# Optimization experiments

Measured on AMD Instinct MI355X. Metric: run time of the kernel, lower is better.

The kernel has to match this reference:

```python
import jax, jax.numpy as jnp
import numpy as np

B, L, S, N, D, DT, V, H = 32, 256, 5, 1024, 256, 256, 512, 8
Dh = D // H


def layernorm(x, g, b, eps=1e-5):
    m = x.mean(-1, keepdims=True)
    v = ((x - m) ** 2).mean(-1, keepdims=True)
    return (x - m) / jnp.sqrt(v + eps) * g + b


def setup_inputs() -> dict:
    key = jax.random.key(0)
    ks = jax.random.split(key, 16)
    sc = lambda k, shape: jax.random.normal(k, shape, jnp.float32) * 0.02
    return {
        'vis_tokens': jax.random.normal(ks[0], (B, N, D), jnp.float32),
        'left_ctx_ids': jax.random.randint(ks[1], (B, L, S), 0, V),
        'right_ctx_ids': jax.random.randint(ks[2], (B, L, S), 0, V),
        'tgt_ids': jax.random.randint(ks[3], (B, L), 0, V),
        'tgt_mask': jnp.ones((B, L), jnp.float32),
        'vis_mask': jax.random.uniform(ks[4], (B, L, N), jnp.float32),
        'emb_w': sc(ks[5], (V, DT)),          # tied embedding / classifier weight
        'dir_left': sc(ks[6], (DT,)),
        'dir_right': sc(ks[7], (DT,)),
        'txt_proj_w': sc(ks[8], (D, DT)), 'txt_proj_b': jnp.zeros((D,), jnp.float32),
        'q_gamma': jnp.ones((D,), jnp.float32), 'q_beta': jnp.zeros((D,), jnp.float32),
        'k_w': sc(ks[9], (D, D)), 'k_b': jnp.zeros((D,), jnp.float32),
        'v_w': sc(ks[10], (D, D)), 'v_b': jnp.zeros((D,), jnp.float32),
        'kv_gamma': jnp.ones((D,), jnp.float32), 'kv_beta': jnp.zeros((D,), jnp.float32),
        'tau': jnp.asarray(1.0, jnp.float32),
        'cls_b': jnp.zeros((V,), jnp.float32),
        'conv_w_l': sc(ks[11], (DT, DT, 3)),   # fresh random conv weight per call in torch
        'conv_w_r': sc(ks[12], (DT, DT, 3)),
    }


def _ctx_to_query(ctx_ids, dir_tok, conv_w, emb_w, txt_proj_w, txt_proj_b, qg, qb):
    E = emb_w[ctx_ids]                                    # [B,L,S,DT]
    q = jnp.transpose(E, (0, 1, 3, 2)).reshape(B * L, DT, S)
    q = jax.lax.conv_general_dilated(q, conv_w, (1,), [(1, 1)],
                                     dimension_numbers=('NCH', 'OIH', 'NCH'))  # [B*L,DT,S]
    # faithful to torch: flat reinterpretation [B*L,DT,S] -> [B,L,S,DT], then mean over dim 2
    q = q.reshape(B, L, -1, DT).mean(2)                   # [B,L,DT]
    q = q + dir_tok
    return layernorm(q @ txt_proj_w.T + txt_proj_b, qg, qb)  # [B,L,D]


def _cross_attend(Q, Fv, vis_mask, k_w, k_b, v_w, v_b, kvg, kvb, tau):
    K = layernorm(Fv @ k_w.T + k_b, kvg, kvb)             # [B,N,D]
    Vv = layernorm(Fv @ v_w.T + v_b, kvg, kvb)
    q = Q.reshape(B, L, H, Dh).transpose(0, 2, 1, 3)      # [B,H,L,Dh]
    k = K.reshape(B, N, H, Dh).transpose(0, 2, 1, 3)
    v = Vv.reshape(B, N, H, Dh).transpose(0, 2, 1, 3)
    tau_c = jnp.clip(tau, 0.25, 4.0)
    scores = jnp.einsum('bhld,bhnd->bhln', q, k) / (Dh ** 0.5 * tau_c)
    scores = scores * vis_mask[:, None]                   # multiplicative mask
    attn = jax.nn.softmax(scores, axis=-1)                # dropout = identity (eval)
    out = jnp.einsum('bhln,bhnd->bhld', attn, v)
    return out.transpose(0, 2, 1, 3).reshape(B, L, D)


def reference(vis_tokens, left_ctx_ids, right_ctx_ids, tgt_ids, tgt_mask, vis_mask,
              emb_w, dir_left, dir_right, txt_proj_w, txt_proj_b, q_gamma, q_beta,
              k_w, k_b, v_w, v_b, kv_gamma, kv_beta, tau, cls_b, conv_w_l, conv_w_r):
    Ql = _ctx_to_query(left_ctx_ids, dir_left, conv_w_l, emb_w, txt_proj_w, txt_proj_b, q_gamma, q_beta)
    Qr = _ctx_to_query(right_ctx_ids, dir_right, conv_w_r, emb_w, txt_proj_w, txt_proj_b, q_gamma, q_beta)
    Fl = _cross_attend(Ql, vis_tokens, vis_mask, k_w, k_b, v_w, v_b, kv_gamma, kv_beta, tau)
    Fr = _cross_attend(Qr, vis_tokens, vis_mask, k_w, k_b, v_w, v_b, kv_gamma, kv_beta, tau)
    logits_l = Fl @ emb_w.T + cls_b                       # tied classifier
    logits_r = Fr @ emb_w.T + cls_b
    p_l = jax.nn.softmax(logits_l / 2.0, axis=-1)
    p_r = jax.nn.softmax(logits_r / 2.0, axis=-1)
    agree = ((p_l[:, :-1, :] - p_r[:, 1:, :]) ** 2).sum(-1)
    denom = jnp.maximum(tgt_mask[:, :-1].sum(), 1.0)
    loss_sgm = 0.1 * (agree * tgt_mask[:, :-1]).sum() / denom
    return loss_sgm, logits_l, logits_r
```

## Files before the change

### kernel.cpp

```cpp
#include <hip/hip_runtime.h>

typedef __attribute__((ext_vector_type(8))) short short8;
typedef __attribute__((ext_vector_type(4))) short short4v;
typedef __attribute__((ext_vector_type(4))) float f32x4;

__device__ __forceinline__ short f2bf(float x) {
    union { float f; unsigned u; } c; c.f = x;
    unsigned u = c.u;
    u += 0x7fffu + ((u >> 16) & 1u);
    return (short)(u >> 16);
}

__global__ __launch_bounds__(256) void cvt_bf16(const float* __restrict__ s, short* __restrict__ d, int n4) {
    int i = blockIdx.x * 256 + threadIdx.x;
    if (i < n4) {
        float4 v = ((const float4*)s)[i];
        short4 o;
        o.x = f2bf(v.x); o.y = f2bf(v.y); o.z = f2bf(v.z); o.w = f2bf(v.w);
        ((short4*)d)[i] = o;
    }
}

__global__ __launch_bounds__(256) void cvt3(const float* __restrict__ emb, const float* __restrict__ kw,
                                            const float* __restrict__ vw,
                                            short* __restrict__ de, short* __restrict__ dk, short* __restrict__ dv) {
    int i = blockIdx.x * 256 + threadIdx.x;
    const float* s; short* d; int off;
    if (i < 32768) { s = emb; d = de; off = i; }
    else if (i < 49152) { s = kw; d = dk; off = i - 32768; }
    else { s = vw; d = dv; off = i - 49152; }
    float4 v = ((const float4*)s)[off];
    short4 o;
    o.x = f2bf(v.x); o.y = f2bf(v.y); o.z = f2bf(v.z); o.w = f2bf(v.w);
    ((short4*)d)[off] = o;
}

__global__ void build_wfold(const float* __restrict__ cl, const float* __restrict__ cr,
                            float* __restrict__ wfT) {
    const float* conv_w = blockIdx.y ? cr : cl;
    float* o = wfT + (long)blockIdx.y * 327680;
    const int j = blockIdx.x;
    const int ci = threadIdx.x;
    float acc[5] = {0.f, 0.f, 0.f, 0.f, 0.f};
#pragma unroll
    for (int i = 0; i < 5; ++i) {
        int flat = i * 256 + j;
        int c = flat / 5;
        int s = flat % 5;
#pragma unroll
        for (int k = 0; k < 3; ++k) {
            int si = s + k - 1;
            if (si >= 0 && si < 5) acc[si] += conv_w[(c * 256 + ci) * 3 + k];
        }
    }
#pragma unroll
    for (int si = 0; si < 5; ++si)
        o[(si * 256 + ci) * 256 + j] = acc[si] * 0.2f;
}

template <bool BIAS>
__global__ __launch_bounds__(256) void gemm64(const float* __restrict__ A,
                                              const float* __restrict__ W,
                                              const float* __restrict__ bias,
                                              float* __restrict__ C,
                                              int K, int ldC,
                                              long sliceA, long sliceW, long sliceC) {
    A += (long)blockIdx.z * sliceA;
    W += (long)blockIdx.z * sliceW;
    C += (long)blockIdx.z * sliceC;
    const int row0 = blockIdx.x * 64;
    const int col0 = blockIdx.y * 64;
    __shared__ float As[32][68];
    __shared__ float Ws[32][68];
    const int t = threadIdx.x;
    const int tx = t & 15;
    const int ty = t >> 4;
    float acc[4][4] = {};
    for (int kk = 0; kk < K; kk += 32) {
#pragma unroll
        for (int e = 0; e < 8; ++e) {
            int f = t + 256 * e;
            int r = f >> 5, kc = f & 31;
            As[kc][r] = A[(long)(row0 + r) * K + kk + kc];
            Ws[kc][r] = W[(long)(col0 + r) * K + kk + kc];
        }
        __syncthreads();
#pragma unroll
        for (int kc = 0; kc < 32; ++kc) {
            float4 a4 = *(const float4*)&As[kc][ty * 4];
            float4 w4 = *(const float4*)&Ws[kc][tx * 4];
            float av[4] = {a4.x, a4.y, a4.z, a4.w};
            float wv[4] = {w4.x, w4.y, w4.z, w4.w};
#pragma unroll
            for (int i = 0; i < 4; ++i)
#pragma unroll
                for (int jj = 0; jj < 4; ++jj)
                    acc[i][jj] += av[i] * wv[jj];
        }
        __syncthreads();
    }
#pragma unroll
    for (int r = 0; r < 4; ++r) {
        int row = row0 + ty * 4 + r;
#pragma unroll
        for (int c = 0; c < 4; ++c) {
            int col = col0 + tx * 4 + c;
            float v = acc[r][c];
            if (BIAS) v += bias[col];
            C[(long)row * ldC + col] = v;
        }
    }
}

__global__ __launch_bounds__(256) void gemm_bf(const short* __restrict__ A,
                                               const short* __restrict__ W,
                                               const float* __restrict__ bias,
                                               float* __restrict__ Cf,
                                               int K, int ldC,
                                               long sliceA, long sliceC) {
    A += (long)blockIdx.z * sliceA;
    const int row0 = blockIdx.x * 64, col0 = blockIdx.y * 64;
    __shared__ short As[64 * 40];
    __shared__ short Ws[64 * 40];
    const int t = threadIdx.x;
    const int wid = t >> 6, lane = t & 63, sub = lane & 15, quad = lane >> 4;
    const int wy = wid >> 1, wx = wid & 1;
    const int srow = t >> 2, sseg = t & 3;
    f32x4 acc00 = {0.f, 0.f, 0.f, 0.f}, acc01 = acc00, acc10 = acc00, acc11 = acc00;
    for (int kk = 0; kk < K; kk += 32) {
        *(short8*)&As[srow * 40 + sseg * 8] = *(const short8*)&A[(long)(row0 + srow) * K + kk + sseg * 8];
        *(short8*)&Ws[srow * 40 + sseg * 8] = *(const short8*)&W[(long)(col0 + srow) * K + kk + sseg * 8];
        __syncthreads();
        short8 a0 = *(const short8*)&As[(wy * 32 + sub) * 40 + quad * 8];
        short8 a1 = *(const short8*)&As[(wy * 32 + 16 + sub) * 40 + quad * 8];
        short8 b0 = *(const short8*)&Ws[(wx * 32 + sub) * 40 + quad * 8];
        short8 b1 = *(const short8*)&Ws[(wx * 32 + 16 + sub) * 40 + quad * 8];
        acc00 = __builtin_amdgcn_mfma_f32_16x16x32_bf16(a0, b0, acc00, 0, 0, 0);
        acc01 = __builtin_amdgcn_mfma_f32_16x16x32_bf16(a0, b1, acc01, 0, 0, 0);
        acc10 = __builtin_amdgcn_mfma_f32_16x16x32_bf16(a1, b0, acc10, 0, 0, 0);
        acc11 = __builtin_amdgcn_mfma_f32_16x16x32_bf16(a1, b1, acc11, 0, 0, 0);
        __syncthreads();
    }
    Cf += (long)blockIdx.z * sliceC;
#pragma unroll
    for (int i = 0; i < 2; ++i)
#pragma unroll
        for (int j = 0; j < 2; ++j) {
            f32x4 a = (i == 0) ? (j == 0 ? acc00 : acc01) : (j == 0 ? acc10 : acc11);
#pragma unroll
            for (int r = 0; r < 4; ++r) {
                int row = row0 + wy * 32 + i * 16 + quad * 4 + r;
                int col = col0 + wx * 32 + j * 16 + sub;
                Cf[(long)row * ldC + col] = a[r] + bias[col];
            }
        }
}

__global__ __launch_bounds__(256) void gemm_ln(const short* __restrict__ A,
                                               const short* __restrict__ kwbf, const short* __restrict__ vwbf,
                                               const float* __restrict__ k_b, const float* __restrict__ v_b,
                                               const float* __restrict__ gamma, const float* __restrict__ beta,
                                               short* __restrict__ Kout, short* __restrict__ Vt) {
    const bool isV = blockIdx.y != 0;
    const short* W = isV ? vwbf : kwbf;
    const float* bias = isV ? v_b : k_b;
    const int row0 = blockIdx.x * 64;
    __shared__ short As[64 * 40];
    __shared__ short Ws[256 * 40];
    __shared__ float s_mu[64 * 4];
    __shared__ float s_sq[64 * 4];
    __shared__ float s_mv[64 * 2];
    const int t = threadIdx.x;
    const int wid = t >> 6, lane = t & 63, sub = lane & 15, quad = lane >> 4;
    f32x4 acc[4][4];
#pragma unroll
    for (int mi = 0; mi < 4; ++mi)
#pragma unroll
        for (int ni = 0; ni < 4; ++ni) acc[mi][ni] = (f32x4){0.f, 0.f, 0.f, 0.f};

    const int sr = t >> 2, sseg = t & 3;
    for (int kk = 0; kk < 256; kk += 32) {
        *(short8*)&As[sr * 40 + sseg * 8] = *(const short8*)&A[(long)(row0 + sr) * 256 + kk + sseg * 8];
#pragma unroll
        for (int i = 0; i < 4; ++i) {
            int r = i * 64 + sr;
            *(short8*)&Ws[r * 40 + sseg * 8] = *(const short8*)&W[(long)r * 256 + kk + sseg * 8];
        }
        __syncthreads();
        short8 a[4], b[4];
#pragma unroll
        for (int mi = 0; mi < 4; ++mi) a[mi] = *(const short8*)&As[(mi * 16 + sub) * 40 + quad * 8];
#pragma unroll
        for (int ni = 0; ni < 4; ++ni) b[ni] = *(const short8*)&Ws[(wid * 64 + ni * 16 + sub) * 40 + quad * 8];
#pragma unroll
        for (int mi = 0; mi < 4; ++mi)
#pragma unroll
            for (int ni = 0; ni < 4; ++ni)
                acc[mi][ni] = __builtin_amdgcn_mfma_f32_16x16x32_bf16(a[mi], b[ni], acc[mi][ni], 0, 0, 0);
        __syncthreads();
    }
#pragma unroll
    for (int ni = 0; ni < 4; ++ni) {
        float bv = bias[wid * 64 + ni * 16 + sub];
#pragma unroll
        for (int mi = 0; mi < 4; ++mi)
#pragma unroll
            for (int r = 0; r < 4; ++r) acc[mi][ni][r] += bv;
    }
#pragma unroll
    for (int mi = 0; mi < 4; ++mi) {
#pragma unroll
        for (int r = 0; r < 4; ++r) {
            float s = 0.f, q2 = 0.f;
#pragma unroll
            for (int ni = 0; ni < 4; ++ni) {
                float v = acc[mi][ni][r];
                s += v; q2 += v * v;
            }
#pragma unroll
            for (int off = 8; off; off >>= 1) {
                s += __shfl_xor(s, off, 16);
                q2 += __shfl_xor(q2, off, 16);
            }
            if (sub == 0) {
                int row = mi * 16 + quad * 4 + r;
                s_mu[row * 4 + wid] = s;
                s_sq[row * 4 + wid] = q2;
            }
        }
    }
    __syncthreads();
    if (t < 64) {
        float s = s_mu[t * 4] + s_mu[t * 4 + 1] + s_mu[t * 4 + 2] + s_mu[t * 4 + 3];
        float q2 = s_sq[t * 4] + s_sq[t * 4 + 1] + s_sq[t * 4 + 2] + s_sq[t * 4 + 3];
        float mean = s * (1.0f / 256.0f);
        float var = q2 * (1.0f / 256.0f) - mean * mean;
        s_mv[t * 2] = mean;
        s_mv[t * 2 + 1] = rsqrtf(var + 1e-5f);
    }
    __syncthreads();
#pragma unroll
    for (int ni = 0; ni < 4; ++ni) {
        int col = wid * 64 + ni * 16 + sub;
        float g = gamma[col], bb = beta[col];
        if (!isV) {
#pragma unroll
            for (int mi = 0; mi < 4; ++mi)
#pragma unroll
                for (int r = 0; r < 4; ++r) {
                    int row = mi * 16 + quad * 4 + r;
                    float v = (acc[mi][ni][r] - s_mv[row * 2]) * s_mv[row * 2 + 1] * g + bb;
                    Kout[(long)(row0 + row) * 256 + col] = f2bf(v);
                }
        } else {
            int h = col >> 5, dh = col & 31;
#pragma unroll
            for (int mi = 0; mi < 4; ++mi) {
                int rowb = row0 + mi * 16 + quad * 4;
                short4 o;
#pragma unroll
                for (int r = 0; r < 4; ++r) {
                    int row = mi * 16 + quad * 4 + r;
                    float v = (acc[mi][ni][r] - s_mv[row * 2]) * s_mv[row * 2 + 1] * g + bb;
                    ((short*)&o)[r] = f2bf(v);
                }
                int gb = rowb >> 10, n = rowb & 1023;
                *(short4*)&Vt[((long)(gb * 8 + h) * 32 + dh) * 1024 + n] = o;
            }
        }
    }
}

__global__ void bias_dir_kernel(const float* __restrict__ tp, const float* __restrict__ tpb,
                                const float* __restrict__ dirL, const float* __restrict__ dirR,
                                float* __restrict__ biasL, float* __restrict__ biasR) {
    const float* dir = blockIdx.x ? dirR : dirL;
    float* outp = blockIdx.x ? biasR : biasL;
    __shared__ float sdir[256];
    const int d = threadIdx.x;
    sdir[d] = dir[d];
    __syncthreads();
    float acc = tpb[d];
    for (int j = 0; j < 256; ++j) acc += tp[d * 256 + j] * sdir[j];
    outp[d] = acc;
}

__global__ __launch_bounds__(256) void q_build(const int* __restrict__ idsL, const int* __restrict__ idsR,
                                               const float* __restrict__ Pp,
                                               const float* __restrict__ biasL, const float* __restrict__ biasR,
                                               const float* __restrict__ qg, const float* __restrict__ qb,
                                               short* __restrict__ Qbf) {
    const int wid = threadIdx.x >> 6, lane = threadIdx.x & 63;
    const int bl = blockIdx.x * 4 + wid;
    const bool right = blockIdx.y != 0;
    const int* ids = right ? idsR : idsL;
    const float* P = right ? Pp + 655360 : Pp;
    const float* bias = right ? biasR : biasL;
    const int d0 = lane * 4;
    float4 acc = *(const float4*)&bias[d0];
#pragma unroll
    for (int s = 0; s < 5; ++s) {
        int tok = ids[bl * 5 + s];
        float4 p = *(const float4*)&P[(long)(s * 512 + tok) * 256 + d0];
        acc.x += p.x; acc.y += p.y; acc.z += p.z; acc.w += p.w;
    }
    float sum = acc.x + acc.y + acc.z + acc.w;
    float sq = acc.x * acc.x + acc.y * acc.y + acc.z * acc.z + acc.w * acc.w;
#pragma unroll
    for (int off = 32; off; off >>= 1) {
        sum += __shfl_xor(sum, off, 64);
        sq += __shfl_xor(sq, off, 64);
    }
    float mean = sum * (1.0f / 256.0f);
    float var = sq * (1.0f / 256.0f) - mean * mean;
    float rstd = rsqrtf(var + 1e-5f);
    float4 g = *(const float4*)&qg[d0];
    float4 bb = *(const float4*)&qb[d0];
    short4 o;
    o.x = f2bf((acc.x - mean) * rstd * g.x + bb.x);
    o.y = f2bf((acc.y - mean) * rstd * g.y + bb.y);
    o.z = f2bf((acc.z - mean) * rstd * g.z + bb.z);
    o.w = f2bf((acc.w - mean) * rstd * g.w + bb.w);
    *(short4*)&Qbf[(right ? 2097152L : 0L) + (long)bl * 256 + d0] = o;
}

__device__ __forceinline__ void proc_chunk(
    short8 ak0, short8 ak1, short4v v00, short4v v01, short4v v10, short4v v11,
    const float* __restrict__ mbase, int n0, float inv2,
    const short8 (&bqL)[4], const short8 (&bqR)[4],
    f32x4 (&oL)[4][2], f32x4 (&oR)[4][2], float (&psL)[4], float (&psR)[4]) {
    short8 av0, av1;
#pragma unroll
    for (int j = 0; j < 4; ++j) {
        av0[j] = v00[j]; av0[4 + j] = v01[j];
        av1[j] = v10[j]; av1[4 + j] = v11[j];
    }
#pragma unroll
    for (int lt = 0; lt < 4; ++lt) {
        float4 mk0 = *(const float4*)&mbase[lt * 16384 + n0];
        float4 mk1 = *(const float4*)&mbase[lt * 16384 + n0 + 16];
        float m0x = mk0.x * inv2, m0y = mk0.y * inv2, m0z = mk0.z * inv2, m0w = mk0.w * inv2;
        float m1x = mk1.x * inv2, m1y = mk1.y * inv2, m1z = mk1.z * inv2, m1w = mk1.w * inv2;
        {
            f32x4 c0 = {0.f, 0.f, 0.f, 0.f}, c1 = c0;
            c0 = __builtin_amdgcn_mfma_f32_16x16x32_bf16(ak0, bqL[lt], c0, 0, 0, 0);
            c1 = __builtin_amdgcn_mfma_f32_16x16x32_bf16(ak1, bqL[lt], c1, 0, 0, 0);
            float p0 = __builtin_amdgcn_exp2f(c0[0] * m0x);
            float p1 = __builtin_amdgcn_exp2f(c0[1] * m0y);
            float p2 = __builtin_amdgcn_exp2f(c0[2] * m0z);
            float p3 = __builtin_amdgcn_exp2f(c0[3] * m0w);
            float p4 = __builtin_amdgcn_exp2f(c1[0] * m1x);
            float p5 = __builtin_amdgcn_exp2f(c1[1] * m1y);
            float p6 = __builtin_amdgcn_exp2f(c1[2] * m1z);
            float p7 = __builtin_amdgcn_exp2f(c1[3] * m1w);
            psL[lt] += ((p0 + p1) + (p2 + p3)) + ((p4 + p5) + (p6 + p7));
            short8 p8;
            p8[0] = f2bf(p0); p8[1] = f2bf(p1); p8[2] = f2bf(p2); p8[3] = f2bf(p3);
            p8[4] = f2bf(p4); p8[5] = f2bf(p5); p8[6] = f2bf(p6); p8[7] = f2bf(p7);
            oL[lt][0] = __builtin_amdgcn_mfma_f32_16x16x32_bf16(av0, p8, oL[lt][0], 0, 0, 0);
            oL[lt][1] = __builtin_amdgcn_mfma_f32_16x16x32_bf16(av1, p8, oL[lt][1], 0, 0, 0);
        }
        {
            f32x4 c0 = {0.f, 0.f, 0.f, 0.f}, c1 = c0;
            c0 = __builtin_amdgcn_mfma_f32_16x16x32_bf16(ak0, bqR[lt], c0, 0, 0, 0);
            c1 = __builtin_amdgcn_mfma_f32_16x16x32_bf16(ak1, bqR[lt], c1, 0, 0, 0);
            float p0 = __builtin_amdgcn_exp2f(c0[0] * m0x);
            float p1 = __builtin_amdgcn_exp2f(c0[1] * m0y);
            float p2 = __builtin_amdgcn_exp2f(c0[2] * m0z);
            float p3 = __builtin_amdgcn_exp2f(c0[3] * m0w);
            float p4 = __builtin_amdgcn_exp2f(c1[0] * m1x);
            float p5 = __builtin_amdgcn_exp2f(c1[1] * m1y);
            float p6 = __builtin_amdgcn_exp2f(c1[2] * m1z);
            float p7 = __builtin_amdgcn_exp2f(c1[3] * m1w);
            psR[lt] += ((p0 + p1) + (p2 + p3)) + ((p4 + p5) + (p6 + p7));
            short8 p8;
            p8[0] = f2bf(p0); p8[1] = f2bf(p1); p8[2] = f2bf(p2); p8[3] = f2bf(p3);
            p8[4] = f2bf(p4); p8[5] = f2bf(p5); p8[6] = f2bf(p6); p8[7] = f2bf(p7);
            oR[lt][0] = __builtin_amdgcn_mfma_f32_16x16x32_bf16(av0, p8, oR[lt][0], 0, 0, 0);
            oR[lt][1] = __builtin_amdgcn_mfma_f32_16x16x32_bf16(av1, p8, oR[lt][1], 0, 0, 0);
        }
    }
}

__global__ __launch_bounds__(256, 2) void attn_wave(const short* __restrict__ Qbf,
                                                    const short* __restrict__ Kbf,
                                                    const short* __restrict__ Vt,
                                                    const float* __restrict__ vis_mask,
                                                    const float* __restrict__ tau_p,
                                                    short* __restrict__ Fbf) {
    const int t = threadIdx.x;
    const int wid = t >> 6, lane = t & 63, sub = lane & 15, quad = lane >> 4;
    const int gb = ((blockIdx.x & 7) << 6) | (blockIdx.x >> 3);
    const int b = gb >> 4;
    const int lb = (gb >> 2) & 3;
    const int hp = gb & 3;
    const int wh = wid >> 1, nh = wid & 1;
    const int h = hp * 2 + wh;
    const int l0 = lb * 64;
    float tau = fminf(fmaxf(tau_p[0], 0.25f), 4.0f);
    const float inv2 = 1.4426950408889634f / (5.656854249492381f * tau);

    short8 bqL[4], bqR[4];
#pragma unroll
    for (int lt = 0; lt < 4; ++lt) {
        const long qoff = (long)(b * 256 + l0 + lt * 16 + sub) * 256 + h * 32 + quad * 8;
        bqL[lt] = *(const short8*)&Qbf[qoff];
        bqR[lt] = *(const short8*)&Qbf[2097152 + qoff];
    }

    const short* Kb = Kbf + (long)b * 262144 + h * 32;
    const short* Vb = Vt + (long)(b * 8 + h) * 32768;
    const float* mbase = vis_mask + (long)(b * 256 + l0 + sub) * 1024 + quad * 4;

    f32x4 oL[4][2], oR[4][2];
    float psL[4], psR[4];
#pragma unroll
    for (int lt = 0; lt < 4; ++lt) {
        oL[lt][0] = (f32x4){0.f, 0.f, 0.f, 0.f}; oL[lt][1] = oL[lt][0];
        oR[lt][0] = oL[lt][0]; oR[lt][1] = oL[lt][0];
        psL[lt] = 0.f; psR[lt] = 0.f;
    }

    const int nbeg = nh << 9;

#define LOADK(A0, A1, N)                                                      \
    A0 = *(const short8*)&Kb[(long)((N) + sub) * 256 + quad * 8];             \
    A1 = *(const short8*)&Kb[(long)((N) + 16 + sub) * 256 + quad * 8];
#define LOADV(W00, W01, W10, W11, N)                                          \
    W00 = *(const short4v*)&Vb[(long)sub * 1024 + (N) + quad * 4];            \
    W01 = *(const short4v*)&Vb[(long)sub * 1024 + (N) + 16 + quad * 4];       \
    W10 = *(const short4v*)&Vb[(long)(16 + sub) * 1024 + (N) + quad * 4];     \
    W11 = *(const short4v*)&Vb[(long)(16 + sub) * 1024 + (N) + 16 + quad * 4];

    short8 ak0A, ak1A, ak0B, ak1B;
    short4v v00A, v01A, v10A, v11A, v00B, v01B, v10B, v11B;
    LOADK(ak0A, ak1A, nbeg)
    LOADV(v00A, v01A, v10A, v11A, nbeg)
#pragma unroll 1
    for (int it = 0; it < 8; ++it) {
        const int n0 = nbeg + it * 64;
        LOADK(ak0B, ak1B, n0 + 32)
        LOADV(v00B, v01B, v10B, v11B, n0 + 32)
        proc_chunk(ak0A, ak1A, v00A, v01A, v10A, v11A, mbase, n0, inv2,
                   bqL, bqR, oL, oR, psL, psR);
        const int nx = (it < 7) ? n0 + 64 : nbeg;
        LOADK(ak0A, ak1A, nx)
        LOADV(v00A, v01A, v10A, v11A, nx)
        proc_chunk(ak0B, ak1B, v00B, v01B, v10B, v11B, mbase, n0 + 32, inv2,
                   bqL, bqR, oL, oR, psL, psR);
    }
#undef LOADK
#undef LOADV

#pragma unroll
    for (int lt = 0; lt < 4; ++lt) {
        psL[lt] += __shfl_xor(psL[lt], 16, 64); psL[lt] += __shfl_xor(psL[lt], 32, 64);
        psR[lt] += __shfl_xor(psR[lt], 16, 64); psR[lt] += __shfl_xor(psR[lt], 32, 64);
    }

    __shared__ float red[2][64][72];
    if (nh == 1) {
        float* p = &red[wh][lane][0];
#pragma unroll
        for (int lt = 0; lt < 4; ++lt) {
            *(f32x4*)(p + lt * 8) = oL[lt][0];
            *(f32x4*)(p + lt * 8 + 4) = oL[lt][1];
            *(f32x4*)(p + 32 + lt * 8) = oR[lt][0];
            *(f32x4*)(p + 32 + lt * 8 + 4) = oR[lt][1];
            p[64 + lt] = psL[lt];
            p[68 + lt] = psR[lt];
        }
    }
    __syncthreads();
    if (nh == 1) return;
    {
        const float* p = &red[wh][lane][0];
#pragma unroll
        for (int lt = 0; lt < 4; ++lt) {
            f32x4 e0 = *(const f32x4*)(p + lt * 8);
            f32x4 e1 = *(const f32x4*)(p + lt * 8 + 4);
            f32x4 e2 = *(const f32x4*)(p + 32 + lt * 8);
            f32x4 e3 = *(const f32x4*)(p + 32 + lt * 8 + 4);
#pragma unroll
            for (int r = 0; r < 4; ++r) {
                oL[lt][0][r] += e0[r]; oL[lt][1][r] += e1[r];
                oR[lt][0][r] += e2[r]; oR[lt][1][r] += e3[r];
            }
            psL[lt] += p[64 + lt];
            psR[lt] += p[68 + lt];
        }
    }

#pragma unroll
    for (int lt = 0; lt < 4; ++lt) {
        const long fo = (long)(b * 256 + l0 + lt * 16 + sub) * 256 + h * 32 + quad * 4;
        const float rL = 1.0f / psL[lt], rR = 1.0f / psR[lt];
        short4v s0, s1;
#pragma unroll
        for (int r = 0; r < 4; ++r) { s0[r] = f2bf(oL[lt][0][r] * rL); s1[r] = f2bf(oL[lt][1][r] * rL); }
        *(short4v*)&Fbf[fo] = s0;
        *(short4v*)&Fbf[fo + 16] = s1;
#pragma unroll
        for (int r = 0; r < 4; ++r) { s0[r] = f2bf(oR[lt][0][r] * rR); s1[r] = f2bf(oR[lt][1][r] * rR); }
        *(short4v*)&Fbf[2097152 + fo] = s0;
        *(short4v*)&Fbf[2097152 + fo + 16] = s1;
    }
}

__global__ __launch_bounds__(256) void loss_pair(const float* __restrict__ logits,
                                                 const float* __restrict__ tgt_mask,
                                                 float* __restrict__ partials) {
    const int wid = threadIdx.x >> 6, lane = threadIdx.x & 63;
    const int pid = blockIdx.x * 4 + wid;
    const int b = pid / 255, l = pid - b * 255;
    const float* ll = logits + (long)(b * 256 + l) * 512;
    const float* lr = logits + 4194304 + (long)(b * 256 + l + 1) * 512;
    float a[8], c[8];
#pragma unroll
    for (int j = 0; j < 8; ++j) {
        a[j] = ll[lane + 64 * j] * 0.5f;
        c[j] = lr[lane + 64 * j] * 0.5f;
    }
    float ml = -1e30f, mr = -1e30f;
#pragma unroll
    for (int j = 0; j < 8; ++j) { ml = fmaxf(ml, a[j]); mr = fmaxf(mr, c[j]); }
#pragma unroll
    for (int off = 32; off; off >>= 1) {
        ml = fmaxf(ml, __shfl_xor(ml, off, 64));
        mr = fmaxf(mr, __shfl_xor(mr, off, 64));
    }
    float sl = 0.f, sr = 0.f;
#pragma unroll
    for (int j = 0; j < 8; ++j) {
        a[j] = __expf(a[j] - ml); sl += a[j];
        c[j] = __expf(c[j] - mr); sr += c[j];
    }
#pragma unroll
    for (int off = 32; off; off >>= 1) {
        sl += __shfl_xor(sl, off, 64);
        sr += __shfl_xor(sr, off, 64);
    }
    float rl = 1.0f / sl, rr = 1.0f / sr;
    float sq = 0.f;
#pragma unroll
    for (int j = 0; j < 8; ++j) {
        float d = a[j] * rl - c[j] * rr;
        sq += d * d;
    }
#pragma unroll
    for (int off = 32; off; off >>= 1) sq += __shfl_xor(sq, off, 64);

    __shared__ float sred[4];
    if (lane == 0) sred[wid] = sq * tgt_mask[b * 256 + l];
    __syncthreads();
    if (threadIdx.x == 0)
        partials[blockIdx.x] = (sred[0] + sred[1]) + (sred[2] + sred[3]);
}

__global__ __launch_bounds__(256) void loss_final(const float* __restrict__ tgt_mask,
                                                  const float* __restrict__ partials,
                                                  float* __restrict__ outp) {
    const int t = threadIdx.x;
    float s = 0.f, acc = 0.f;
    for (int i = t; i < 32 * 255; i += 256) {
        int b = i / 255, l = i % 255;
        s += tgt_mask[b * 256 + l];
    }
    for (int i = t; i < 2040; i += 256) acc += partials[i];
    __shared__ float red[256];
    __shared__ float reda[256];
    red[t] = s;
    reda[t] = acc;
    __syncthreads();
    for (int st = 128; st; st >>= 1) {
        if (t < st) { red[t] += red[t + st]; reda[t] += reda[t + st]; }
        __syncthreads();
    }
    if (t == 0) outp[0] = 0.1f * reda[0] / fmaxf(red[0], 1.0f);
}

extern "C" void kernel_launch(void* const* d_in, const int* in_sizes, int n_in,
                              void* d_out, int out_size, void* d_ws, size_t ws_size,
                              hipStream_t stream) {
    const float* vis_tokens = (const float*)d_in[0];
    const int* idsL = (const int*)d_in[1];
    const int* idsR = (const int*)d_in[2];
    const float* tgt_mask = (const float*)d_in[4];
    const float* vis_mask = (const float*)d_in[5];
    const float* emb_w = (const float*)d_in[6];
    const float* dirL = (const float*)d_in[7];
    const float* dirR = (const float*)d_in[8];
    const float* tp_w = (const float*)d_in[9];
    const float* tp_b = (const float*)d_in[10];
    const float* q_g = (const float*)d_in[11];
    const float* q_b = (const float*)d_in[12];
    const float* k_w = (const float*)d_in[13];
    const float* k_b = (const float*)d_in[14];
    const float* v_w = (const float*)d_in[15];
    const float* v_b = (const float*)d_in[16];
    const float* kv_g = (const float*)d_in[17];
    const float* kv_b = (const float*)d_in[18];
    const float* tau = (const float*)d_in[19];
    const float* cls_b = (const float*)d_in[20];
    const float* conv_l = (const float*)d_in[21];
    const float* conv_r = (const float*)d_in[22];
    float* out = (float*)d_out;

    short* sws = (short*)d_ws;
    short* visbf = sws;
    short* embbf = visbf + 8388608;
    short* kwbf  = embbf + 131072;
    short* vwbf  = kwbf + 65536;
    short* Kbf   = vwbf + 65536;
    short* Vt    = Kbf + 8388608;
    short* Qbf   = Vt + 8388608;
    short* Fbf   = Qbf + 4194304;
    float* wfT   = (float*)(Fbf + 4194304);
    float* Ms    = wfT + 655360;
    float* Pp    = Ms + 655360;
    float* bias_l = Pp + 1310720;
    float* bias_r = bias_l + 256;
    float* partials = bias_r + 256;

    cvt_bf16<<<8192, 256, 0, stream>>>(vis_tokens, visbf, 2097152);
    cvt3<<<256, 256, 0, stream>>>(emb_w, k_w, v_w, embbf, kwbf, vwbf);

    build_wfold<<<dim3(256, 2), 256, 0, stream>>>(conv_l, conv_r, wfT);
    gemm64<false><<<dim3(4, 4, 10), 256, 0, stream>>>(tp_w, wfT, nullptr, Ms, 256, 256, 0, 65536, 65536);
    gemm64<false><<<dim3(8, 4, 10), 256, 0, stream>>>(emb_w, Ms, nullptr, Pp, 256, 256, 0, 65536, 131072);
    bias_dir_kernel<<<2, 256, 0, stream>>>(tp_w, tp_b, dirL, dirR, bias_l, bias_r);
    q_build<<<dim3(2048, 2), 256, 0, stream>>>(idsL, idsR, Pp, bias_l, bias_r, q_g, q_b, Qbf);

    gemm_ln<<<dim3(512, 2), 256, 0, stream>>>(visbf, kwbf, vwbf, k_b, v_b, kv_g, kv_b, Kbf, Vt);

    attn_wave<<<512, 256, 0, stream>>>(Qbf, Kbf, Vt, vis_mask, tau, Fbf);

    gemm_bf<<<dim3(128, 8, 2), 256, 0, stream>>>(Fbf, embbf, cls_b, out + 1, 256, 512,
                                                 2097152, 4194304);

    loss_pair<<<2040, 256, 0, stream>>>(out + 1, tgt_mask, partials);
    loss_final<<<1, 256, 0, stream>>>(tgt_mask, partials, out);
}
```

Before: 359.5 us.

## Stage vis_mask through swizzled LDS double buffer with 4-head 512-thread blocks

The attention kernel now uses 512-thread blocks that cover four heads instead of two, so each vis_mask tile is loaded once per block and shared by more heads. The mask is prefetched into a double-buffered, XOR-swizzled shared-memory buffer, overlapped with compute, and each wave reads its slice from LDS instead of issuing scattered global float4 loads. This cuts redundant global mask traffic across heads. In exchange it adds two block-wide barriers per iteration and more shared memory, and the block count halves to one block per CU.

```diff
diff --git a/kernel.cpp b/kernel.cpp
--- a/kernel.cpp
+++ b/kernel.cpp
@@ -326,7 +326,7 @@
 
 __device__ __forceinline__ void proc_chunk(
     short8 ak0, short8 ak1, short4v v00, short4v v01, short4v v10, short4v v11,
-    const float* __restrict__ mbase, int n0, float inv2,
+    const float* mlds, int sub, int quad, float inv2,
     const short8 (&bqL)[4], const short8 (&bqR)[4],
     f32x4 (&oL)[4][2], f32x4 (&oR)[4][2], float (&psL)[4], float (&psR)[4]) {
     short8 av0, av1;
@@ -335,10 +335,12 @@
         av0[j] = v00[j]; av0[4 + j] = v01[j];
         av1[j] = v10[j]; av1[4 + j] = v11[j];
     }
+    const int sw = (quad ^ (sub & 7)) << 2;
 #pragma unroll
     for (int lt = 0; lt < 4; ++lt) {
-        float4 mk0 = *(const float4*)&mbase[lt * 16384 + n0];
-        float4 mk1 = *(const float4*)&mbase[lt * 16384 + n0 + 16];
+        const int mi = ((lt * 16 + sub) << 5) + sw;
+        float4 mk0 = *(const float4*)&mlds[mi];
+        float4 mk1 = *(const float4*)&mlds[mi ^ 16];
         float m0x = mk0.x * inv2, m0y = mk0.y * inv2, m0z = mk0.z * inv2, m0w = mk0.w * inv2;
         float m1x = mk1.x * inv2, m1y = mk1.y * inv2, m1z = mk1.z * inv2, m1w = mk1.w * inv2;
         {
@@ -382,7 +384,7 @@
     }
 }
 
-__global__ __launch_bounds__(256, 2) void attn_wave(const short* __restrict__ Qbf,
+__global__ __launch_bounds__(512, 1) void attn_wave(const short* __restrict__ Qbf,
                                                     const short* __restrict__ Kbf,
                                                     const short* __restrict__ Vt,
                                                     const float* __restrict__ vis_mask,
@@ -390,15 +392,26 @@
                                                     short* __restrict__ Fbf) {
     const int t = threadIdx.x;
     const int wid = t >> 6, lane = t & 63, sub = lane & 15, quad = lane >> 4;
-    const int gb = ((blockIdx.x & 7) << 6) | (blockIdx.x >> 3);
-    const int b = gb >> 4;
-    const int lb = (gb >> 2) & 3;
-    const int hp = gb & 3;
+    const int gb = ((blockIdx.x & 7) << 5) | (blockIdx.x >> 3);
+    const int b = gb >> 3;
+    const int lb = (gb >> 1) & 3;
+    const int hq = gb & 1;
     const int wh = wid >> 1, nh = wid & 1;
-    const int h = hp * 2 + wh;
+    const int h = hq * 4 + wh;
     const int l0 = lb * 64;
     float tau = fminf(fmaxf(tau_p[0], 0.25f), 4.0f);
     const float inv2 = 1.4426950408889634f / (5.656854249492381f * tau);
+
+    __shared__ float mbuf[2 * 4096];
+    __shared__ float red[4][64][72];
+
+    const int s0 = t * 2;
+    const int l_s = (s0 >> 3) & 63, nh_s = s0 >> 9;
+    const int n4a = s0 & 7, n4b = n4a + 1;
+    const float* mrow0 = vis_mask + (long)(b * 256 + l0 + l_s) * 1024 + nh_s * 512 + 4 * (n4a ^ (l_s & 7));
+    const float* mrow1 = vis_mask + (long)(b * 256 + l0 + l_s) * 1024 + nh_s * 512 + 4 * (n4b ^ (l_s & 7));
+    float* mdst0 = mbuf + nh_s * 2048 + l_s * 32 + n4a * 4;
+    float* mdst1 = mbuf + nh_s * 2048 + l_s * 32 + n4b * 4;
 
     short8 bqL[4], bqR[4];
 #pragma unroll
@@ -410,7 +423,7 @@
 
     const short* Kb = Kbf + (long)b * 262144 + h * 32;
     const short* Vb = Vt + (long)(b * 8 + h) * 32768;
-    const float* mbase = vis_mask + (long)(b * 256 + l0 + sub) * 1024 + quad * 4;
+    const float* mld = mbuf + nh * 2048;
 
     f32x4 oL[4][2], oR[4][2];
     float psL[4], psR[4];
@@ -434,20 +447,44 @@
 
     short8 ak0A, ak1A, ak0B, ak1B;
     short4v v00A, v01A, v10A, v11A, v00B, v01B, v10B, v11B;
+    float4 mr0, mr1;
+
+    mr0 = *(const float4*)&mrow0[0];
+    mr1 = *(const float4*)&mrow1[0];
+    *(float4*)&mdst0[0] = mr0;
+    *(float4*)&mdst1[0] = mr1;
     LOADK(ak0A, ak1A, nbeg)
     LOADV(v00A, v01A, v10A, v11A, nbeg)
+    __syncthreads();
+
 #pragma unroll 1
-    for (int it = 0; it < 8; ++it) {
-        const int n0 = nbeg + it * 64;
+    for (int j = 0; j < 8; ++j) {
+        const int n0 = nbeg + j * 64;
         LOADK(ak0B, ak1B, n0 + 32)
         LOADV(v00B, v01B, v10B, v11B, n0 + 32)
-        proc_chunk(ak0A, ak1A, v00A, v01A, v10A, v11A, mbase, n0, inv2,
+        {
+            const int nrel = j * 64 + 32;
+            mr0 = *(const float4*)&mrow0[nrel];
+            mr1 = *(const float4*)&mrow1[nrel];
+        }
+        proc_chunk(ak0A, ak1A, v00A, v01A, v10A, v11A, mld, sub, quad, inv2,
                    bqL, bqR, oL, oR, psL, psR);
-        const int nx = (it < 7) ? n0 + 64 : nbeg;
+        *(float4*)&mdst0[4096] = mr0;
+        *(float4*)&mdst1[4096] = mr1;
+        __syncthreads();
+        const int nx = (j < 7) ? n0 + 64 : nbeg;
         LOADK(ak0A, ak1A, nx)
         LOADV(v00A, v01A, v10A, v11A, nx)
-        proc_chunk(ak0B, ak1B, v00B, v01B, v10B, v11B, mbase, n0 + 32, inv2,
+        {
+            const int nrel = (j < 7) ? j * 64 + 64 : 0;
+            mr0 = *(const float4*)&mrow0[nrel];
+            mr1 = *(const float4*)&mrow1[nrel];
+        }
+        proc_chunk(ak0B, ak1B, v00B, v01B, v10B, v11B, mld + 4096, sub, quad, inv2,
                    bqL, bqR, oL, oR, psL, psR);
+        *(float4*)&mdst0[0] = mr0;
+        *(float4*)&mdst1[0] = mr1;
+        __syncthreads();
     }
 #undef LOADK
 #undef LOADV
@@ -458,7 +495,6 @@
         psR[lt] += __shfl_xor(psR[lt], 16, 64); psR[lt] += __shfl_xor(psR[lt], 32, 64);
     }
 
-    __shared__ float red[2][64][72];
     if (nh == 1) {
         float* p = &red[wh][lane][0];
 #pragma unroll
@@ -495,15 +531,15 @@
     for (int lt = 0; lt < 4; ++lt) {
         const long fo = (long)(b * 256 + l0 + lt * 16 + sub) * 256 + h * 32 + quad * 4;
         const float rL = 1.0f / psL[lt], rR = 1.0f / psR[lt];
-        short4v s0, s1;
-#pragma unroll
-        for (int r = 0; r < 4; ++r) { s0[r] = f2bf(oL[lt][0][r] * rL); s1[r] = f2bf(oL[lt][1][r] * rL); }
-        *(short4v*)&Fbf[fo] = s0;
-        *(short4v*)&Fbf[fo + 16] = s1;
-#pragma unroll
-        for (int r = 0; r < 4; ++r) { s0[r] = f2bf(oR[lt][0][r] * rR); s1[r] = f2bf(oR[lt][1][r] * rR); }
-        *(short4v*)&Fbf[2097152 + fo] = s0;
-        *(short4v*)&Fbf[2097152 + fo + 16] = s1;
+        short4v s0v, s1v;
+#pragma unroll
+        for (int r = 0; r < 4; ++r) { s0v[r] = f2bf(oL[lt][0][r] * rL); s1v[r] = f2bf(oL[lt][1][r] * rL); }
+        *(short4v*)&Fbf[fo] = s0v;
+        *(short4v*)&Fbf[fo + 16] = s1v;
+#pragma unroll
+        for (int r = 0; r < 4; ++r) { s0v[r] = f2bf(oR[lt][0][r] * rR); s1v[r] = f2bf(oR[lt][1][r] * rR); }
+        *(short4v*)&Fbf[2097152 + fo] = s0v;
+        *(short4v*)&Fbf[2097152 + fo + 16] = s1v;
     }
 }
 
@@ -633,7 +669,7 @@
 
     gemm_ln<<<dim3(512, 2), 256, 0, stream>>>(visbf, kwbf, vwbf, k_b, v_b, kv_g, kv_b, Kbf, Vt);
 
-    attn_wave<<<512, 256, 0, stream>>>(Qbf, Kbf, Vt, vis_mask, tau, Fbf);
+    attn_wave<<<256, 512, 0, stream>>>(Qbf, Kbf, Vt, vis_mask, tau, Fbf);
 
     gemm_bf<<<dim3(128, 8, 2), 256, 0, stream>>>(Fbf, embbf, cls_b, out + 1, 256, 512,
                                                  2097152, 4194304);
```

Result: faster. 334.5 us (-7.0%).
